# Performance work log

Measured on AMD Instinct MI355X. Metric: run time of the kernel, lower is better.

## Reference

```python
import jax, jax.numpy as jnp
import numpy as np

# Layer dims and sparsity levels, hard-coded in the original module
_DIMS = [(1024, 1000, 0.73), (1000, 800, 0.72), (800, 400, 0.70), (400, 600, 0.70), (600, 6, 0.50)]


def setup_inputs() -> dict:
    key = jax.random.key(0)
    ks = jax.random.split(key, 1 + 3 * len(_DIMS))
    inp = {"x": jax.random.normal(ks[0], (32768, 1024), dtype=jnp.float32)}
    for i, (fin, fout, sp) in enumerate(_DIMS):
        kw, kb, km = ks[1 + 3 * i], ks[2 + 3 * i], ks[3 + 3 * i]
        # Kaiming-ish init like nn.Linear default
        bound = 1.0 / np.sqrt(fin)
        inp[f"W{i+1}"] = jax.random.uniform(kw, (fout, fin), jnp.float32, -bound, bound)
        inp[f"b{i+1}"] = jax.random.uniform(kb, (fout,), jnp.float32, -bound, bound)
        # Unstructured sparsity mask: fraction `sp` of weights are zero
        inp[f"mask{i+1}"] = (jax.random.uniform(km, (fout, fin)) >= sp)
    return inp


def _sparse_linear(x, W, b, mask):
    # y = x @ (W * mask)^T + b ; mask encodes the fixed sparse connectivity
    Ws = jnp.where(mask, W, 0.0)
    return x @ Ws.T + b


def reference(x, W1, b1, mask1, W2, b2, mask2, W3, b3, mask3, W4, b4, mask4, W5, b5, mask5):
    h1 = jax.nn.relu(_sparse_linear(x, W1, b1, mask1))   # [B, 1000]
    h2 = jax.nn.relu(_sparse_linear(h1, W2, b2, mask2))  # [B, 800]
    h3 = jax.nn.relu(_sparse_linear(h2, W3, b3, mask3))  # [B, 400]
    h4 = _sparse_linear(h3, W4, b4, mask4)               # [B, 600] (no relu)
    h5 = _sparse_linear(h4, W5, b5, mask5)               # [B, 6]   (no relu)
    # original returns (x, results dict); return tuple (final, fc1..fc5)
    return (h5, h1, h2, h3, h4, h5)
```

## Files before the change

kernel.cpp:

```cpp
#include <hip/hip_runtime.h>
#include <stdint.h>

using u8  = unsigned char;
using u16 = unsigned short;
using u32 = unsigned int;

typedef __bf16 bf16x8 __attribute__((ext_vector_type(8)));
typedef float  f32x4  __attribute__((ext_vector_type(4)));
typedef u16    u16x8  __attribute__((ext_vector_type(8)));

__device__ __forceinline__ float b2f(u16 u) {
    union { u32 i; float f; } v; v.i = ((u32)u) << 16; return v.f;
}
__device__ __forceinline__ u16 f2bf(float f) {
    union { float f; u32 i; } v; v.f = f;
    u32 u = v.i;
    return (u16)((u + 0x7FFFu + ((u >> 16) & 1u)) >> 16);
}

#define WS_OFF 256
#define OFF_W1 0
#define OFF_W2 1048576
#define OFF_W3 1966080
#define OFF_W4 2392064
#define PS1 1048576
#define PS2 917504
#define PS3 425984
#define PS4 286720
#define TOTW 2678784
#define GUARD 64
#define OFF_XC  2678784
#define OFF_H1C 36233216
#define OFF_H2C 69001280
#define OFF_H3C 95215744
#define XCONV_N 4194304

__global__ void detect_kernel(int* __restrict__ flags,
                              const u32* __restrict__ xw,
                              const u32* __restrict__ mw) {
    const int lane = threadIdx.x;
    int outl = 0;
#pragma unroll
    for (int i = 0; i < 4; ++i) {
        u32 u = xw[lane * 4 + i];
        u32 e = (u >> 7) & 0xFFu;
        if (e < 90u || e > 140u) outl++;
    }
#pragma unroll
    for (int off = 32; off; off >>= 1) outl += __shfl_down(outl, off, 64);

    u32 v0 = mw[lane], v1 = mw[64 + lane];
    bool w4 = (v0 == 0u || v0 == 1u || v0 == 0x3F800000u) &&
              (v1 == 0u || v1 == 1u || v1 == 0x3F800000u);
    auto okh = [](u32 h) { return h == 0u || h == 1u || h == 0x3F80u; };
    bool w2 = okh(v0 & 0xFFFFu) && okh(v0 >> 16) && okh(v1 & 0xFFFFu) && okh(v1 >> 16);
    int all4 = __all(w4 ? 1 : 0);
    int all2 = __all(w2 ? 1 : 0);
    if (lane == 0) {
        flags[0] = (outl > 64) ? 1 : 0;
        flags[1] = all4 ? 0 : (all2 ? 1 : 2);
    }
}

__device__ __forceinline__ bool readM(const void* m, int s, int mwid) {
    if (mwid == 0) return ((const u32*)m)[s] != 0u;
    if (mwid == 1) return ((const u16*)m)[s] != 0u;
    return ((const u8*)m)[s] != 0u;
}
__device__ __forceinline__ u16 readW(const void* W, int s, int dt) {
    if (dt) return f2bf(((const float*)W)[s]);
    return ((const u16*)W)[s];
}

__global__ void prep_weights(const int* __restrict__ flags, u16* __restrict__ ws,
                             const void* __restrict__ W1, const void* __restrict__ m1,
                             const void* __restrict__ W2, const void* __restrict__ m2,
                             const void* __restrict__ W3, const void* __restrict__ m3,
                             const void* __restrict__ W4, const void* __restrict__ m4,
                             const void* __restrict__ xv)
{
    const int dt = flags[0], mwid = flags[1];
    int idx = blockIdx.x * 256 + threadIdx.x;
    if (idx < PS1) {
        int n = idx >> 10, k = idx & 1023;
        u16 v = 0;
        if (n < 1000) { int s = n * 1024 + k; if (readM(m1, s, mwid)) v = readW(W1, s, dt); }
        ws[idx] = v;
    } else if (idx < PS1 + PS2) {
        int j = idx - PS1; int n = j >> 10, k = j & 1023;
        u16 v = 0;
        if (n < 800 && k < 1000) { int s = n * 1000 + k; if (readM(m2, s, mwid)) v = readW(W2, s, dt); }
        ws[idx] = v;
    } else if (idx < PS1 + PS2 + PS3) {
        int j = idx - (PS1 + PS2); int n = j / 832, k = j - n * 832;
        u16 v = 0;
        if (n < 400 && k < 800) { int s = n * 800 + k; if (readM(m3, s, mwid)) v = readW(W3, s, dt); }
        ws[idx] = v;
    } else if (idx < TOTW) {
        int j = idx - (PS1 + PS2 + PS3); int n = j / 448, k = j - n * 448;
        u16 v = 0;
        if (n < 600 && k < 400) { int s = n * 400 + k; if (readM(m4, s, mwid)) v = readW(W4, s, dt); }
        ws[idx] = v;
    } else if (idx < TOTW + 3 * GUARD) {
        int g = idx - TOTW;
        int zone = g >> 6;
        size_t off = (zone == 0) ? ((size_t)OFF_H1C + 32768000)
                   : (zone == 1) ? ((size_t)OFF_H2C + 26214400)
                                 : ((size_t)OFF_H3C + 13107200);
        ws[off + (g & 63)] = 0;
    } else if (dt) {
        int c = idx - (TOTW + 3 * GUARD);
        if (c < XCONV_N) {
            const float4* s = (const float4*)xv + (size_t)c * 2;
            float4 a = s[0], b = s[1];
            u16x8 o;
            o[0] = f2bf(a.x); o[1] = f2bf(a.y); o[2] = f2bf(a.z); o[3] = f2bf(a.w);
            o[4] = f2bf(b.x); o[5] = f2bf(b.y); o[6] = f2bf(b.z); o[7] = f2bf(b.w);
            ((u16x8*)(ws + OFF_XC))[c] = o;
        }
    }
}

template <bool RELU>
__global__ __launch_bounds__(256, 3) void gemm_bt(
    const int* __restrict__ flags,
    const u16* __restrict__ A0,
    const u16* __restrict__ A1,
    int strideA, int Kpad, int NY,
    const u16* __restrict__ Wp,
    const void* __restrict__ bias, int N,
    void* __restrict__ dOut, size_t outOff,
    u16* __restrict__ Cc)
{
    const int mode = flags[0];
    const u16* __restrict__ A = mode ? A1 : A0;

    __shared__ __attribute__((aligned(16))) char sA[16384];
    __shared__ __attribute__((aligned(16))) char sB[16384];

    const int tid  = threadIdx.x;
    const int lane = tid & 63, wid = tid >> 6;
    const int wm = wid >> 1, wn = wid & 1;

    const int per = gridDim.x >> 3;
    const int idx = (blockIdx.x & 7) * per + (blockIdx.x >> 3);
    const int bm0 = (idx / NY) * 128, bn0 = (idx % NY) * 128;

    const int q = lane >> 4, r15 = lane & 15, key = lane & 7;
    const int l3 = lane >> 3, l7 = lane & 7;
    const int kbx = (l7 ^ l3) << 3;

    const u16* gA = A  + (size_t)(bm0 + wid * 32 + l3) * (size_t)strideA + kbx;
    const u16* gB = Wp + (size_t)(bn0 + wid * 32 + l3) * (size_t)Kpad   + kbx;
    char* sAw = sA + wid * 4096;
    char* sBw = sB + wid * 4096;

    f32x4 acc[4][4];
#pragma unroll
    for (int i = 0; i < 4; ++i)
#pragma unroll
        for (int j = 0; j < 4; ++j) acc[i][j] = (f32x4){0.f, 0.f, 0.f, 0.f};

    for (int k0 = 0; k0 < Kpad; k0 += 64) {
        if (k0) __syncthreads();
#pragma unroll
        for (int t = 0; t < 4; ++t) {
            __builtin_amdgcn_global_load_lds(
                (const __attribute__((address_space(1))) void*)(gA + (size_t)t * 8 * strideA),
                (__attribute__((address_space(3))) void*)(sAw + t * 1024), 16, 0, 0);
            __builtin_amdgcn_global_load_lds(
                (const __attribute__((address_space(1))) void*)(gB + (size_t)t * 8 * Kpad),
                (__attribute__((address_space(3))) void*)(sBw + t * 1024), 16, 0, 0);
        }
        gA += 64; gB += 64;
        __syncthreads();

#pragma unroll
        for (int kk = 0; kk < 2; ++kk) {
            bf16x8 af[4], bfr[4];
#pragma unroll
            for (int mi = 0; mi < 4; ++mi)
                af[mi] = *(const bf16x8*)(sA + (wm * 64 + mi * 16 + r15) * 128 +
                                          (((kk * 4 + q) ^ key) << 4));
#pragma unroll
            for (int ni = 0; ni < 4; ++ni)
                bfr[ni] = *(const bf16x8*)(sB + (wn * 64 + ni * 16 + r15) * 128 +
                                           (((kk * 4 + q) ^ key) << 4));
#pragma unroll
            for (int mi = 0; mi < 4; ++mi)
#pragma unroll
                for (int ni = 0; ni < 4; ++ni)
                    acc[mi][ni] = __builtin_amdgcn_mfma_f32_16x16x32_bf16(
                        af[mi], bfr[ni], acc[mi][ni], 0, 0, 0);
        }
    }

    float bv[4];
#pragma unroll
    for (int ni = 0; ni < 4; ++ni) {
        int col = bn0 + wn * 64 + ni * 16 + r15;
        bv[ni] = (col < N) ? (mode ? ((const float*)bias)[col] : b2f(((const u16*)bias)[col]))
                           : 0.f;
    }
    float* out32 = (float*)dOut + outOff;
    u16*   out16 = (u16*)dOut + outOff;
#pragma unroll
    for (int mi = 0; mi < 4; ++mi) {
#pragma unroll
        for (int ni = 0; ni < 4; ++ni) {
            int col = bn0 + wn * 64 + ni * 16 + r15;
            if (col < N) {
#pragma unroll
                for (int rr = 0; rr < 4; ++rr) {
                    int row = bm0 + wm * 64 + mi * 16 + q * 4 + rr;
                    float v = acc[mi][ni][rr] + bv[ni];
                    if (RELU) v = v > 0.f ? v : 0.f;
                    size_t o = (size_t)row * N + col;
                    if (Cc) Cc[o] = f2bf(v);
                    if (mode) out32[o] = v;
                    else      out16[o] = f2bf(v);
                }
            }
        }
    }
}

__global__ void layer5(const int* __restrict__ flags, void* __restrict__ dOut,
                       const void* __restrict__ W5v, const void* __restrict__ b5v,
                       const void* __restrict__ m5v)
{
    const int mode = flags[0], mwid = flags[1];
    __shared__ float w[6 * 600];
    __shared__ float bs[6];
    const int tid = threadIdx.x;
    for (int i = tid; i < 3600; i += 256)
        w[i] = readM(m5v, i, mwid)
                 ? (mode ? ((const float*)W5v)[i] : b2f(((const u16*)W5v)[i])) : 0.f;
    if (tid < 6)
        bs[tid] = mode ? ((const float*)b5v)[tid] : b2f(((const u16*)b5v)[tid]);
    __syncthreads();

    const int wid = tid >> 6, lane = tid & 63;
    const int row = blockIdx.x * 4 + wid;

    const float* h4f = (const float*)dOut + 72286208;
    const u16*   h4b = (const u16*)dOut + 72286208;

    float acc[6] = {0.f, 0.f, 0.f, 0.f, 0.f, 0.f};
    for (int p = lane; p < 300; p += 64) {
        float f0, f1;
        if (mode) {
            float2 hv = *(const float2*)(h4f + (size_t)row * 600 + 2 * p);
            f0 = hv.x; f1 = hv.y;
        } else {
            u32 u = *(const u32*)(h4b + (size_t)row * 600 + 2 * p);
            f0 = b2f((u16)(u & 0xffff)); f1 = b2f((u16)(u >> 16));
        }
        int k = 2 * p;
#pragma unroll
        for (int j = 0; j < 6; ++j) {
            float2 wv = *(const float2*)&w[j * 600 + k];
            acc[j] += f0 * wv.x + f1 * wv.y;
        }
    }
#pragma unroll
    for (int j = 0; j < 6; ++j)
#pragma unroll
        for (int off = 32; off > 0; off >>= 1)
            acc[j] += __shfl_down(acc[j], off, 64);

    if (lane == 0) {
#pragma unroll
        for (int j = 0; j < 6; ++j) {
            float v = acc[j] + bs[j];
            size_t o0 = (size_t)row * 6 + j;
            if (mode) {
                ((float*)dOut)[o0] = v;
                ((float*)dOut)[91947008 + o0] = v;
            } else {
                u16 b = f2bf(v);
                ((u16*)dOut)[o0] = b;
                ((u16*)dOut)[91947008 + o0] = b;
            }
        }
    }
}

extern "C" void kernel_launch(void* const* d_in, const int* in_sizes, int n_in,
                              void* d_out, int out_size, void* d_ws, size_t ws_size,
                              hipStream_t stream) {
    int* flags = (int*)d_ws;
    u16* wsW   = (u16*)d_ws + WS_OFF;

    detect_kernel<<<1, 64, 0, stream>>>(flags, (const u32*)d_in[0], (const u32*)d_in[3]);
    prep_weights<<<26849, 256, 0, stream>>>(flags, wsW,
                                            d_in[1], d_in[3], d_in[4], d_in[6],
                                            d_in[7], d_in[9], d_in[10], d_in[12],
                                            d_in[0]);

    gemm_bt<true><<<2048, 256, 0, stream>>>(flags, (const u16*)d_in[0], wsW + OFF_XC,
                                            1024, 1024, 8, wsW + OFF_W1, d_in[2], 1000,
                                            d_out, 196608, wsW + OFF_H1C);
    gemm_bt<true><<<1792, 256, 0, stream>>>(flags, wsW + OFF_H1C, wsW + OFF_H1C,
                                            1000, 1024, 7, wsW + OFF_W2, d_in[5], 800,
                                            d_out, 32964608, wsW + OFF_H2C);
    gemm_bt<true><<<1024, 256, 0, stream>>>(flags, wsW + OFF_H2C, wsW + OFF_H2C,
                                            800, 832, 4, wsW + OFF_W3, d_in[8], 400,
                                            d_out, 59179008, wsW + OFF_H3C);
    gemm_bt<false><<<1280, 256, 0, stream>>>(flags, wsW + OFF_H3C, wsW + OFF_H3C,
                                             400, 448, 5, wsW + OFF_W4, d_in[11], 600,
                                             d_out, 72286208, (u16*)nullptr);
    layer5<<<8192, 256, 0, stream>>>(flags, d_out, d_in[13], d_in[14], d_in[15]);
}
```

Measured before the change: 826.9 us.

## Fuse layer-5 projection into layer-4 GEMM epilogue with atomic partial sums

Layer 5 (600->6) is now computed inside the layer-4 GEMM epilogue. Each block multiplies its output tile by the matching slice of W5 held in shared memory, reduces across lanes, and atomically adds partial sums into a zeroed fp32 scratch buffer. A small finalize kernel then adds the bias and writes both copies of h5. This avoids re-reading h4 from global memory in a separate kernel. It adds atomics and an extra shared-memory fill in the epilogue, and launch bounds are raised from 3 to 4 blocks per SM, which may cause register spills.

```diff
diff --git a/kernel.cpp b/kernel.cpp
--- a/kernel.cpp
+++ b/kernel.cpp
@@ -33,6 +33,8 @@
 #define OFF_H1C 36233216
 #define OFF_H2C 69001280
 #define OFF_H3C 95215744
+#define OFF_H5S 108323008
+#define H5N 196608
 #define XCONV_N 4194304
 
 __global__ void detect_kernel(int* __restrict__ flags,
@@ -108,8 +110,10 @@
                    : (zone == 1) ? ((size_t)OFF_H2C + 26214400)
                                  : ((size_t)OFF_H3C + 13107200);
         ws[off + (g & 63)] = 0;
+    } else if (idx < TOTW + 3 * GUARD + H5N) {
+        ((float*)(ws + OFF_H5S))[idx - (TOTW + 3 * GUARD)] = 0.f;
     } else if (dt) {
-        int c = idx - (TOTW + 3 * GUARD);
+        int c = idx - (TOTW + 3 * GUARD + H5N);
         if (c < XCONV_N) {
             const float4* s = (const float4*)xv + (size_t)c * 2;
             float4 a = s[0], b = s[1];
@@ -121,8 +125,8 @@
     }
 }
 
-template <bool RELU>
-__global__ __launch_bounds__(256, 3) void gemm_bt(
+template <bool RELU, bool FUSE>
+__global__ __launch_bounds__(256, 4) void gemm_bt(
     const int* __restrict__ flags,
     const u16* __restrict__ A0,
     const u16* __restrict__ A1,
@@ -130,7 +134,9 @@
     const u16* __restrict__ Wp,
     const void* __restrict__ bias, int N,
     void* __restrict__ dOut, size_t outOff,
-    u16* __restrict__ Cc)
+    u16* __restrict__ Cc,
+    const void* __restrict__ W5v, const void* __restrict__ m5v,
+    float* __restrict__ scratch)
 {
     const int mode = flags[0];
     const u16* __restrict__ A = mode ? A1 : A0;
@@ -195,6 +201,21 @@
         }
     }
 
+    float* w5s = (float*)sA;
+    if constexpr (FUSE) {
+        const int mwid = flags[1];
+        __syncthreads();
+        for (int i = tid; i < 768; i += 256) {
+            int j = i >> 7, c = i & 127, col = bn0 + c;
+            float wv = 0.f;
+            if (col < 600 && readM(m5v, j * 600 + col, mwid))
+                wv = mode ? ((const float*)W5v)[j * 600 + col]
+                          : b2f(((const u16*)W5v)[j * 600 + col]);
+            w5s[i] = wv;
+        }
+        __syncthreads();
+    }
+
     float bv[4];
 #pragma unroll
     for (int ni = 0; ni < 4; ++ni) {
@@ -202,87 +223,68 @@
         bv[ni] = (col < N) ? (mode ? ((const float*)bias)[col] : b2f(((const u16*)bias)[col]))
                            : 0.f;
     }
+    float wreg[6][4];
+    if constexpr (FUSE) {
+#pragma unroll
+        for (int j = 0; j < 6; ++j)
+#pragma unroll
+            for (int ni = 0; ni < 4; ++ni)
+                wreg[j][ni] = w5s[j * 128 + wn * 64 + ni * 16 + r15];
+    }
+
     float* out32 = (float*)dOut + outOff;
     u16*   out16 = (u16*)dOut + outOff;
 #pragma unroll
     for (int mi = 0; mi < 4; ++mi) {
 #pragma unroll
-        for (int ni = 0; ni < 4; ++ni) {
-            int col = bn0 + wn * 64 + ni * 16 + r15;
-            if (col < N) {
-#pragma unroll
-                for (int rr = 0; rr < 4; ++rr) {
-                    int row = bm0 + wm * 64 + mi * 16 + q * 4 + rr;
-                    float v = acc[mi][ni][rr] + bv[ni];
-                    if (RELU) v = v > 0.f ? v : 0.f;
+        for (int rr = 0; rr < 4; ++rr) {
+            int row = bm0 + wm * 64 + mi * 16 + q * 4 + rr;
+            float vv[4];
+#pragma unroll
+            for (int ni = 0; ni < 4; ++ni) {
+                float v = acc[mi][ni][rr] + bv[ni];
+                if (RELU) v = v > 0.f ? v : 0.f;
+                vv[ni] = v;
+                int col = bn0 + wn * 64 + ni * 16 + r15;
+                if (col < N) {
                     size_t o = (size_t)row * N + col;
                     if (Cc) Cc[o] = f2bf(v);
                     if (mode) out32[o] = v;
                     else      out16[o] = f2bf(v);
                 }
             }
-        }
-    }
-}
-
-__global__ void layer5(const int* __restrict__ flags, void* __restrict__ dOut,
-                       const void* __restrict__ W5v, const void* __restrict__ b5v,
-                       const void* __restrict__ m5v)
+            if constexpr (FUSE) {
+#pragma unroll
+                for (int j = 0; j < 6; ++j) {
+                    float p = vv[0] * wreg[j][0] + vv[1] * wreg[j][1] +
+                              vv[2] * wreg[j][2] + vv[3] * wreg[j][3];
+                    p += __shfl_xor(p, 1, 64);
+                    p += __shfl_xor(p, 2, 64);
+                    p += __shfl_xor(p, 4, 64);
+                    p += __shfl_xor(p, 8, 64);
+                    if (r15 == 0) atomicAdd(&scratch[(size_t)row * 6 + j], p);
+                }
+            }
+        }
+    }
+}
+
+__global__ void finalize5(const int* __restrict__ flags,
+                          const float* __restrict__ scratch,
+                          const void* __restrict__ b5v, void* __restrict__ dOut)
 {
-    const int mode = flags[0], mwid = flags[1];
-    __shared__ float w[6 * 600];
-    __shared__ float bs[6];
-    const int tid = threadIdx.x;
-    for (int i = tid; i < 3600; i += 256)
-        w[i] = readM(m5v, i, mwid)
-                 ? (mode ? ((const float*)W5v)[i] : b2f(((const u16*)W5v)[i])) : 0.f;
-    if (tid < 6)
-        bs[tid] = mode ? ((const float*)b5v)[tid] : b2f(((const u16*)b5v)[tid]);
-    __syncthreads();
-
-    const int wid = tid >> 6, lane = tid & 63;
-    const int row = blockIdx.x * 4 + wid;
-
-    const float* h4f = (const float*)dOut + 72286208;
-    const u16*   h4b = (const u16*)dOut + 72286208;
-
-    float acc[6] = {0.f, 0.f, 0.f, 0.f, 0.f, 0.f};
-    for (int p = lane; p < 300; p += 64) {
-        float f0, f1;
-        if (mode) {
-            float2 hv = *(const float2*)(h4f + (size_t)row * 600 + 2 * p);
-            f0 = hv.x; f1 = hv.y;
-        } else {
-            u32 u = *(const u32*)(h4b + (size_t)row * 600 + 2 * p);
-            f0 = b2f((u16)(u & 0xffff)); f1 = b2f((u16)(u >> 16));
-        }
-        int k = 2 * p;
-#pragma unroll
-        for (int j = 0; j < 6; ++j) {
-            float2 wv = *(const float2*)&w[j * 600 + k];
-            acc[j] += f0 * wv.x + f1 * wv.y;
-        }
-    }
-#pragma unroll
-    for (int j = 0; j < 6; ++j)
-#pragma unroll
-        for (int off = 32; off > 0; off >>= 1)
-            acc[j] += __shfl_down(acc[j], off, 64);
-
-    if (lane == 0) {
-#pragma unroll
-        for (int j = 0; j < 6; ++j) {
-            float v = acc[j] + bs[j];
-            size_t o0 = (size_t)row * 6 + j;
-            if (mode) {
-                ((float*)dOut)[o0] = v;
-                ((float*)dOut)[91947008 + o0] = v;
-            } else {
-                u16 b = f2bf(v);
-                ((u16*)dOut)[o0] = b;
-                ((u16*)dOut)[91947008 + o0] = b;
-            }
-        }
+    const int mode = flags[0];
+    int idx = blockIdx.x * 256 + threadIdx.x;
+    int j = idx % 6;
+    float v = scratch[idx] +
+              (mode ? ((const float*)b5v)[j] : b2f(((const u16*)b5v)[j]));
+    if (mode) {
+        ((float*)dOut)[idx] = v;
+        ((float*)dOut)[91947008 + idx] = v;
+    } else {
+        u16 b = f2bf(v);
+        ((u16*)dOut)[idx] = b;
+        ((u16*)dOut)[91947008 + idx] = b;
     }
 }
 
@@ -291,24 +293,29 @@
                               hipStream_t stream) {
     int* flags = (int*)d_ws;
     u16* wsW   = (u16*)d_ws + WS_OFF;
+    float* h5s = (float*)(wsW + OFF_H5S);
 
     detect_kernel<<<1, 64, 0, stream>>>(flags, (const u32*)d_in[0], (const u32*)d_in[3]);
-    prep_weights<<<26849, 256, 0, stream>>>(flags, wsW,
+    prep_weights<<<27617, 256, 0, stream>>>(flags, wsW,
                                             d_in[1], d_in[3], d_in[4], d_in[6],
                                             d_in[7], d_in[9], d_in[10], d_in[12],
                                             d_in[0]);
 
-    gemm_bt<true><<<2048, 256, 0, stream>>>(flags, (const u16*)d_in[0], wsW + OFF_XC,
-                                            1024, 1024, 8, wsW + OFF_W1, d_in[2], 1000,
-                                            d_out, 196608, wsW + OFF_H1C);
-    gemm_bt<true><<<1792, 256, 0, stream>>>(flags, wsW + OFF_H1C, wsW + OFF_H1C,
-                                            1000, 1024, 7, wsW + OFF_W2, d_in[5], 800,
-                                            d_out, 32964608, wsW + OFF_H2C);
-    gemm_bt<true><<<1024, 256, 0, stream>>>(flags, wsW + OFF_H2C, wsW + OFF_H2C,
-                                            800, 832, 4, wsW + OFF_W3, d_in[8], 400,
-                                            d_out, 59179008, wsW + OFF_H3C);
-    gemm_bt<false><<<1280, 256, 0, stream>>>(flags, wsW + OFF_H3C, wsW + OFF_H3C,
-                                             400, 448, 5, wsW + OFF_W4, d_in[11], 600,
-                                             d_out, 72286208, (u16*)nullptr);
-    layer5<<<8192, 256, 0, stream>>>(flags, d_out, d_in[13], d_in[14], d_in[15]);
-}
+    gemm_bt<true, false><<<2048, 256, 0, stream>>>(flags, (const u16*)d_in[0], wsW + OFF_XC,
+                                                   1024, 1024, 8, wsW + OFF_W1, d_in[2], 1000,
+                                                   d_out, 196608, wsW + OFF_H1C,
+                                                   nullptr, nullptr, nullptr);
+    gemm_bt<true, false><<<1792, 256, 0, stream>>>(flags, wsW + OFF_H1C, wsW + OFF_H1C,
+                                                   1000, 1024, 7, wsW + OFF_W2, d_in[5], 800,
+                                                   d_out, 32964608, wsW + OFF_H2C,
+                                                   nullptr, nullptr, nullptr);
+    gemm_bt<true, false><<<1024, 256, 0, stream>>>(flags, wsW + OFF_H2C, wsW + OFF_H2C,
+                                                   800, 832, 4, wsW + OFF_W3, d_in[8], 400,
+                                                   d_out, 59179008, wsW + OFF_H3C,
+                                                   nullptr, nullptr, nullptr);
+    gemm_bt<false, true><<<1280, 256, 0, stream>>>(flags, wsW + OFF_H3C, wsW + OFF_H3C,
+                                                   400, 448, 5, wsW + OFF_W4, d_in[11], 600,
+                                                   d_out, 72286208, (u16*)nullptr,
+                                                   d_in[13], d_in[15], h5s);
+    finalize5<<<768, 256, 0, stream>>>(flags, h5s, d_in[14], d_out);
+}
```

Result: slower. 916.1 us (+10.8%).

## Use 256x256 tiles with double-buffered LDS pipeline in GEMM kernels

Applied to the files above, without the earlier changes.

Replaces the 128x128, 4-wave GEMM with a 256x256, 8-wave kernel whose A and B tiles sit in a 128KB double-buffered LDS region. The next K-stage is prefetched with global_load_lds while the current one is consumed, using explicit vmcnt waits and raw barriers instead of __syncthreads. It also raises MFMA priority around the compute block. The aim is more data reuse per tile and overlap of memory with compute. In exchange, the grids are much smaller (256-512 blocks), which may underfill the GPU and waste more work on padded edges for N=1000/800/400/600.

```diff
diff --git a/kernel.cpp b/kernel.cpp
--- a/kernel.cpp
+++ b/kernel.cpp
@@ -8,6 +8,9 @@
 typedef __bf16 bf16x8 __attribute__((ext_vector_type(8)));
 typedef float  f32x4  __attribute__((ext_vector_type(4)));
 typedef u16    u16x8  __attribute__((ext_vector_type(8)));
+
+#define AS1 __attribute__((address_space(1)))
+#define AS3 __attribute__((address_space(3)))
 
 __device__ __forceinline__ float b2f(u16 u) {
     union { u32 i; float f; } v; v.i = ((u32)u) << 16; return v.f;
@@ -122,11 +125,11 @@
 }
 
 template <bool RELU>
-__global__ __launch_bounds__(256, 3) void gemm_bt(
+__global__ __launch_bounds__(512, 2) void gemm256(
     const int* __restrict__ flags,
     const u16* __restrict__ A0,
     const u16* __restrict__ A1,
-    int strideA, int Kpad, int NY,
+    int strideA, int NT, int NY,
     const u16* __restrict__ Wp,
     const void* __restrict__ bias, int N,
     void* __restrict__ dOut, size_t outOff,
@@ -134,64 +137,91 @@
 {
     const int mode = flags[0];
     const u16* __restrict__ A = mode ? A1 : A0;
-
-    __shared__ __attribute__((aligned(16))) char sA[16384];
-    __shared__ __attribute__((aligned(16))) char sB[16384];
+    const int Kpad = NT * 64;
+
+    __shared__ __attribute__((aligned(16))) char smem[131072];
 
     const int tid  = threadIdx.x;
-    const int lane = tid & 63, wid = tid >> 6;
-    const int wm = wid >> 1, wn = wid & 1;
+    const int lane = tid & 63;
+    const int wid  = tid >> 6;
+    const int wm = wid >> 2, wn = wid & 3;
+    const int q = lane >> 4, r15 = lane & 15;
+    const int csq = q ^ ((r15 >> 1) & 3);
 
     const int per = gridDim.x >> 3;
     const int idx = (blockIdx.x & 7) * per + (blockIdx.x >> 3);
-    const int bm0 = (idx / NY) * 128, bn0 = (idx % NY) * 128;
-
-    const int q = lane >> 4, r15 = lane & 15, key = lane & 7;
-    const int l3 = lane >> 3, l7 = lane & 7;
-    const int kbx = (l7 ^ l3) << 3;
-
-    const u16* gA = A  + (size_t)(bm0 + wid * 32 + l3) * (size_t)strideA + kbx;
-    const u16* gB = Wp + (size_t)(bn0 + wid * 32 + l3) * (size_t)Kpad   + kbx;
-    char* sAw = sA + wid * 4096;
-    char* sBw = sB + wid * 4096;
-
-    f32x4 acc[4][4];
-#pragma unroll
-    for (int i = 0; i < 4; ++i)
+    const int bm0 = (idx / NY) * 256, bn0 = (idx % NY) * 256;
+
+    int srA[2], scA[2];
+#pragma unroll
+    for (int l = 0; l < 2; ++l) {
+        int m = l * 512 + tid;
+        int r = m >> 2, c = m & 3;
+        srA[l] = r;
+        scA[l] = (c ^ ((r >> 1) & 3)) * 8;
+    }
+
+    f32x4 acc[8][4];
+#pragma unroll
+    for (int i = 0; i < 8; ++i)
 #pragma unroll
         for (int j = 0; j < 4; ++j) acc[i][j] = (f32x4){0.f, 0.f, 0.f, 0.f};
 
-    for (int k0 = 0; k0 < Kpad; k0 += 64) {
-        if (k0) __syncthreads();
-#pragma unroll
-        for (int t = 0; t < 4; ++t) {
-            __builtin_amdgcn_global_load_lds(
-                (const __attribute__((address_space(1))) void*)(gA + (size_t)t * 8 * strideA),
-                (__attribute__((address_space(3))) void*)(sAw + t * 1024), 16, 0, 0);
-            __builtin_amdgcn_global_load_lds(
-                (const __attribute__((address_space(1))) void*)(gB + (size_t)t * 8 * Kpad),
-                (__attribute__((address_space(3))) void*)(sBw + t * 1024), 16, 0, 0);
-        }
-        gA += 64; gB += 64;
-        __syncthreads();
-
+    auto STAGE = [&](int t, int kk) {
+        const int kb = t * 64 + kk * 32;
+        const int pb = t & 1;
+        char* ldsA = smem + pb * 32768 + kk * 16384;
+        char* ldsB = smem + 65536 + pb * 32768 + kk * 16384;
+#pragma unroll
+        for (int l = 0; l < 2; ++l) {
+            const u16* src = A + (size_t)(bm0 + srA[l]) * (size_t)strideA + kb + scA[l];
+            __builtin_amdgcn_global_load_lds((const AS1 void*)src,
+                (AS3 void*)(ldsA + (l * 512 + tid) * 16), 16, 0, 0);
+        }
+#pragma unroll
+        for (int l = 0; l < 2; ++l) {
+            const u16* src = Wp + (size_t)(bn0 + srA[l]) * (size_t)Kpad + kb + scA[l];
+            __builtin_amdgcn_global_load_lds((const AS1 void*)src,
+                (AS3 void*)(ldsB + (l * 512 + tid) * 16), 16, 0, 0);
+        }
+    };
+
+    STAGE(0, 0);
+    STAGE(0, 1);
+
+    for (int t = 0; t < NT; ++t) {
+        const int pb = t & 1;
 #pragma unroll
         for (int kk = 0; kk < 2; ++kk) {
-            bf16x8 af[4], bfr[4];
-#pragma unroll
-            for (int mi = 0; mi < 4; ++mi)
-                af[mi] = *(const bf16x8*)(sA + (wm * 64 + mi * 16 + r15) * 128 +
-                                          (((kk * 4 + q) ^ key) << 4));
-#pragma unroll
-            for (int ni = 0; ni < 4; ++ni)
-                bfr[ni] = *(const bf16x8*)(sB + (wn * 64 + ni * 16 + r15) * 128 +
-                                           (((kk * 4 + q) ^ key) << 4));
-#pragma unroll
-            for (int mi = 0; mi < 4; ++mi)
+            const bool st = (t + 1 < NT);
+            if (st) STAGE(t + 1, kk);
+            if (st)           asm volatile("s_waitcnt vmcnt(8)" ::: "memory");
+            else if (kk == 0) asm volatile("s_waitcnt vmcnt(4)" ::: "memory");
+            else              asm volatile("s_waitcnt vmcnt(0)" ::: "memory");
+            __builtin_amdgcn_s_barrier();
+            __builtin_amdgcn_sched_barrier(0);
+
+            const char* Ab = smem + pb * 32768 + kk * 16384;
+            const char* Bb = smem + 65536 + pb * 32768 + kk * 16384;
+            bf16x8 af[8], bfr[4];
+#pragma unroll
+            for (int mi = 0; mi < 8; ++mi) {
+                int r = wm * 128 + mi * 16 + r15;
+                af[mi] = *(const bf16x8*)(Ab + r * 64 + csq * 16);
+            }
+#pragma unroll
+            for (int ni = 0; ni < 4; ++ni) {
+                int r = wn * 64 + ni * 16 + r15;
+                bfr[ni] = *(const bf16x8*)(Bb + r * 64 + csq * 16);
+            }
+            __builtin_amdgcn_s_setprio(1);
+#pragma unroll
+            for (int mi = 0; mi < 8; ++mi)
 #pragma unroll
                 for (int ni = 0; ni < 4; ++ni)
                     acc[mi][ni] = __builtin_amdgcn_mfma_f32_16x16x32_bf16(
                         af[mi], bfr[ni], acc[mi][ni], 0, 0, 0);
+            __builtin_amdgcn_s_setprio(0);
         }
     }
 
@@ -205,14 +235,14 @@
     float* out32 = (float*)dOut + outOff;
     u16*   out16 = (u16*)dOut + outOff;
 #pragma unroll
-    for (int mi = 0; mi < 4; ++mi) {
+    for (int mi = 0; mi < 8; ++mi) {
 #pragma unroll
         for (int ni = 0; ni < 4; ++ni) {
             int col = bn0 + wn * 64 + ni * 16 + r15;
             if (col < N) {
 #pragma unroll
                 for (int rr = 0; rr < 4; ++rr) {
-                    int row = bm0 + wm * 64 + mi * 16 + q * 4 + rr;
+                    int row = bm0 + wm * 128 + mi * 16 + q * 4 + rr;
                     float v = acc[mi][ni][rr] + bv[ni];
                     if (RELU) v = v > 0.f ? v : 0.f;
                     size_t o = (size_t)row * N + col;
@@ -298,17 +328,17 @@
                                             d_in[7], d_in[9], d_in[10], d_in[12],
                                             d_in[0]);
 
-    gemm_bt<true><<<2048, 256, 0, stream>>>(flags, (const u16*)d_in[0], wsW + OFF_XC,
-                                            1024, 1024, 8, wsW + OFF_W1, d_in[2], 1000,
-                                            d_out, 196608, wsW + OFF_H1C);
-    gemm_bt<true><<<1792, 256, 0, stream>>>(flags, wsW + OFF_H1C, wsW + OFF_H1C,
-                                            1000, 1024, 7, wsW + OFF_W2, d_in[5], 800,
-                                            d_out, 32964608, wsW + OFF_H2C);
-    gemm_bt<true><<<1024, 256, 0, stream>>>(flags, wsW + OFF_H2C, wsW + OFF_H2C,
-                                            800, 832, 4, wsW + OFF_W3, d_in[8], 400,
-                                            d_out, 59179008, wsW + OFF_H3C);
-    gemm_bt<false><<<1280, 256, 0, stream>>>(flags, wsW + OFF_H3C, wsW + OFF_H3C,
-                                             400, 448, 5, wsW + OFF_W4, d_in[11], 600,
-                                             d_out, 72286208, (u16*)nullptr);
+    gemm256<true><<<512, 512, 0, stream>>>(flags, (const u16*)d_in[0], wsW + OFF_XC,
+                                           1024, 16, 4, wsW + OFF_W1, d_in[2], 1000,
+                                           d_out, 196608, wsW + OFF_H1C);
+    gemm256<true><<<512, 512, 0, stream>>>(flags, wsW + OFF_H1C, wsW + OFF_H1C,
+                                           1000, 16, 4, wsW + OFF_W2, d_in[5], 800,
+                                           d_out, 32964608, wsW + OFF_H2C);
+    gemm256<true><<<256, 512, 0, stream>>>(flags, wsW + OFF_H2C, wsW + OFF_H2C,
+                                           800, 13, 2, wsW + OFF_W3, d_in[8], 400,
+                                           d_out, 59179008, wsW + OFF_H3C);
+    gemm256<false><<<384, 512, 0, stream>>>(flags, wsW + OFF_H3C, wsW + OFF_H3C,
+                                            400, 7, 3, wsW + OFF_W4, d_in[11], 600,
+                                            d_out, 72286208, (u16*)nullptr);
     layer5<<<8192, 256, 0, stream>>>(flags, d_out, d_in[13], d_in[14], d_in[15]);
 }
```

Measured after the change: 812.9 us. No clear change (-1.7%).

## Fuse prep, GEMM layers, and layer5 into one persistent cooperative kernel

Applied to the files above, without the earlier changes.

Replaces the separate prep, four GEMM and layer5 launches with one persistent cooperative kernel. Its blocks loop over tiles in each phase and use grid.sync between phases, with a fallback to the old multi-launch path if the cooperative launch fails. The aim is to remove launch gaps and tail effects between kernels. In exchange it drops the XCD-aware block remapping, keeps the grid fixed at occupancy times CU count, and adds the cost of the grid-wide barriers.

```diff
diff --git a/kernel.cpp b/kernel.cpp
--- a/kernel.cpp
+++ b/kernel.cpp
@@ -1,5 +1,8 @@
 #include <hip/hip_runtime.h>
+#include <hip/hip_cooperative_groups.h>
 #include <stdint.h>
+
+namespace cg = cooperative_groups;
 
 using u8  = unsigned char;
 using u16 = unsigned short;
@@ -8,6 +11,9 @@
 typedef __bf16 bf16x8 __attribute__((ext_vector_type(8)));
 typedef float  f32x4  __attribute__((ext_vector_type(4)));
 typedef u16    u16x8  __attribute__((ext_vector_type(8)));
+
+#define AS1 __attribute__((address_space(1)))
+#define AS3 __attribute__((address_space(3)))
 
 __device__ __forceinline__ float b2f(u16 u) {
     union { u32 i; float f; } v; v.i = ((u32)u) << 16; return v.f;
@@ -34,6 +40,7 @@
 #define OFF_H2C 69001280
 #define OFF_H3C 95215744
 #define XCONV_N 4194304
+#define PREP_TOT (TOTW + 3 * GUARD + XCONV_N)
 
 __global__ void detect_kernel(int* __restrict__ flags,
                               const u32* __restrict__ xw,
@@ -72,15 +79,13 @@
     return ((const u16*)W)[s];
 }
 
-__global__ void prep_weights(const int* __restrict__ flags, u16* __restrict__ ws,
-                             const void* __restrict__ W1, const void* __restrict__ m1,
-                             const void* __restrict__ W2, const void* __restrict__ m2,
-                             const void* __restrict__ W3, const void* __restrict__ m3,
-                             const void* __restrict__ W4, const void* __restrict__ m4,
-                             const void* __restrict__ xv)
-{
-    const int dt = flags[0], mwid = flags[1];
-    int idx = blockIdx.x * 256 + threadIdx.x;
+__device__ __forceinline__ void prep_one(int idx, int dt, int mwid, u16* __restrict__ ws,
+                                         const void* __restrict__ W1, const void* __restrict__ m1,
+                                         const void* __restrict__ W2, const void* __restrict__ m2,
+                                         const void* __restrict__ W3, const void* __restrict__ m3,
+                                         const void* __restrict__ W4, const void* __restrict__ m4,
+                                         const void* __restrict__ xv)
+{
     if (idx < PS1) {
         int n = idx >> 10, k = idx & 1023;
         u16 v = 0;
@@ -122,30 +127,15 @@
 }
 
 template <bool RELU>
-__global__ __launch_bounds__(256, 3) void gemm_bt(
-    const int* __restrict__ flags,
-    const u16* __restrict__ A0,
-    const u16* __restrict__ A1,
-    int strideA, int Kpad, int NY,
-    const u16* __restrict__ Wp,
-    const void* __restrict__ bias, int N,
-    void* __restrict__ dOut, size_t outOff,
-    u16* __restrict__ Cc)
-{
-    const int mode = flags[0];
-    const u16* __restrict__ A = mode ? A1 : A0;
-
-    __shared__ __attribute__((aligned(16))) char sA[16384];
-    __shared__ __attribute__((aligned(16))) char sB[16384];
-
+__device__ __forceinline__ void gemm_tile(
+    int mode, const u16* __restrict__ A, int strideA, int Kpad,
+    const u16* __restrict__ Wp, const void* __restrict__ bias, int N,
+    void* __restrict__ dOut, size_t outOff, u16* __restrict__ Cc,
+    int bm0, int bn0, char* sA, char* sB)
+{
     const int tid  = threadIdx.x;
     const int lane = tid & 63, wid = tid >> 6;
     const int wm = wid >> 1, wn = wid & 1;
-
-    const int per = gridDim.x >> 3;
-    const int idx = (blockIdx.x & 7) * per + (blockIdx.x >> 3);
-    const int bm0 = (idx / NY) * 128, bn0 = (idx % NY) * 128;
-
     const int q = lane >> 4, r15 = lane & 15, key = lane & 7;
     const int l3 = lane >> 3, l7 = lane & 7;
     const int kbx = (l7 ^ l3) << 3;
@@ -161,16 +151,17 @@
 #pragma unroll
         for (int j = 0; j < 4; ++j) acc[i][j] = (f32x4){0.f, 0.f, 0.f, 0.f};
 
+    __syncthreads();
     for (int k0 = 0; k0 < Kpad; k0 += 64) {
         if (k0) __syncthreads();
 #pragma unroll
         for (int t = 0; t < 4; ++t) {
             __builtin_amdgcn_global_load_lds(
-                (const __attribute__((address_space(1))) void*)(gA + (size_t)t * 8 * strideA),
-                (__attribute__((address_space(3))) void*)(sAw + t * 1024), 16, 0, 0);
+                (const AS1 void*)(gA + (size_t)t * 8 * strideA),
+                (AS3 void*)(sAw + t * 1024), 16, 0, 0);
             __builtin_amdgcn_global_load_lds(
-                (const __attribute__((address_space(1))) void*)(gB + (size_t)t * 8 * Kpad),
-                (__attribute__((address_space(3))) void*)(sBw + t * 1024), 16, 0, 0);
+                (const AS1 void*)(gB + (size_t)t * 8 * Kpad),
+                (AS3 void*)(sBw + t * 1024), 16, 0, 0);
         }
         gA += 64; gB += 64;
         __syncthreads();
@@ -225,13 +216,27 @@
     }
 }
 
-__global__ void layer5(const int* __restrict__ flags, void* __restrict__ dOut,
-                       const void* __restrict__ W5v, const void* __restrict__ b5v,
-                       const void* __restrict__ m5v)
-{
-    const int mode = flags[0], mwid = flags[1];
-    __shared__ float w[6 * 600];
-    __shared__ float bs[6];
+template <bool RELU>
+__device__ void gemm_phase(int mode, const u16* __restrict__ A, int strideA, int Kpad,
+                           const u16* __restrict__ Wp, const void* __restrict__ bias,
+                           int N, int nyt, int mtiles,
+                           void* __restrict__ dOut, size_t outOff, u16* __restrict__ Cc,
+                           char* sA, char* sB)
+{
+    const int ntiles = mtiles * nyt;
+    for (int tt = blockIdx.x; tt < ntiles; tt += gridDim.x) {
+        const int mt = tt / nyt, nt = tt - mt * nyt;
+        gemm_tile<RELU>(mode, A, strideA, Kpad, Wp, bias, N,
+                        dOut, outOff, Cc, mt * 128, nt * 128, sA, sB);
+    }
+}
+
+__device__ void layer5_phase(int mode, int mwid, void* __restrict__ dOut,
+                             const void* __restrict__ W5v, const void* __restrict__ b5v,
+                             const void* __restrict__ m5v, char* smem)
+{
+    float* w  = (float*)smem;
+    float* bs = (float*)(smem + 14400);
     const int tid = threadIdx.x;
     for (int i = tid; i < 3600; i += 256)
         w[i] = readM(m5v, i, mwid)
@@ -241,49 +246,126 @@
     __syncthreads();
 
     const int wid = tid >> 6, lane = tid & 63;
-    const int row = blockIdx.x * 4 + wid;
-
     const float* h4f = (const float*)dOut + 72286208;
     const u16*   h4b = (const u16*)dOut + 72286208;
 
-    float acc[6] = {0.f, 0.f, 0.f, 0.f, 0.f, 0.f};
-    for (int p = lane; p < 300; p += 64) {
-        float f0, f1;
-        if (mode) {
-            float2 hv = *(const float2*)(h4f + (size_t)row * 600 + 2 * p);
-            f0 = hv.x; f1 = hv.y;
-        } else {
-            u32 u = *(const u32*)(h4b + (size_t)row * 600 + 2 * p);
-            f0 = b2f((u16)(u & 0xffff)); f1 = b2f((u16)(u >> 16));
-        }
-        int k = 2 * p;
-#pragma unroll
-        for (int j = 0; j < 6; ++j) {
-            float2 wv = *(const float2*)&w[j * 600 + k];
-            acc[j] += f0 * wv.x + f1 * wv.y;
-        }
-    }
-#pragma unroll
-    for (int j = 0; j < 6; ++j)
-#pragma unroll
-        for (int off = 32; off > 0; off >>= 1)
-            acc[j] += __shfl_down(acc[j], off, 64);
-
-    if (lane == 0) {
-#pragma unroll
-        for (int j = 0; j < 6; ++j) {
-            float v = acc[j] + bs[j];
-            size_t o0 = (size_t)row * 6 + j;
+    for (int g = blockIdx.x; g < 8192; g += gridDim.x) {
+        const int row = g * 4 + wid;
+        float acc[6] = {0.f, 0.f, 0.f, 0.f, 0.f, 0.f};
+        for (int p = lane; p < 300; p += 64) {
+            float f0, f1;
             if (mode) {
-                ((float*)dOut)[o0] = v;
-                ((float*)dOut)[91947008 + o0] = v;
+                float2 hv = *(const float2*)(h4f + (size_t)row * 600 + 2 * p);
+                f0 = hv.x; f1 = hv.y;
             } else {
-                u16 b = f2bf(v);
-                ((u16*)dOut)[o0] = b;
-                ((u16*)dOut)[91947008 + o0] = b;
+                u32 u = *(const u32*)(h4b + (size_t)row * 600 + 2 * p);
+                f0 = b2f((u16)(u & 0xffff)); f1 = b2f((u16)(u >> 16));
             }
-        }
-    }
+            int k = 2 * p;
+#pragma unroll
+            for (int j = 0; j < 6; ++j) {
+                float2 wv = *(const float2*)&w[j * 600 + k];
+                acc[j] += f0 * wv.x + f1 * wv.y;
+            }
+        }
+#pragma unroll
+        for (int j = 0; j < 6; ++j)
+#pragma unroll
+            for (int off = 32; off > 0; off >>= 1)
+                acc[j] += __shfl_down(acc[j], off, 64);
+
+        if (lane == 0) {
+#pragma unroll
+            for (int j = 0; j < 6; ++j) {
+                float v = acc[j] + bs[j];
+                size_t o0 = (size_t)row * 6 + j;
+                if (mode) {
+                    ((float*)dOut)[o0] = v;
+                    ((float*)dOut)[91947008 + o0] = v;
+                } else {
+                    u16 b = f2bf(v);
+                    ((u16*)dOut)[o0] = b;
+                    ((u16*)dOut)[91947008 + o0] = b;
+                }
+            }
+        }
+    }
+}
+
+__global__ __launch_bounds__(256, 3) void mega(
+    const int* __restrict__ flags, u16* __restrict__ ws,
+    const void* __restrict__ W1, const void* __restrict__ m1,
+    const void* __restrict__ W2, const void* __restrict__ m2,
+    const void* __restrict__ W3, const void* __restrict__ m3,
+    const void* __restrict__ W4, const void* __restrict__ m4,
+    const void* __restrict__ W5, const void* __restrict__ b5,
+    const void* __restrict__ m5, const void* __restrict__ xv,
+    const void* __restrict__ b1, const void* __restrict__ b2,
+    const void* __restrict__ b3, const void* __restrict__ b4,
+    void* __restrict__ dOut)
+{
+    cg::grid_group grid = cg::this_grid();
+    __shared__ __attribute__((aligned(16))) char smem[32768];
+    const int dt = flags[0], mwid = flags[1];
+    const int stride = gridDim.x * 256;
+
+    for (int idx = blockIdx.x * 256 + threadIdx.x; idx < PREP_TOT; idx += stride)
+        prep_one(idx, dt, mwid, ws, W1, m1, W2, m2, W3, m3, W4, m4, xv);
+    grid.sync();
+
+    {
+        const u16* A = dt ? ws + OFF_XC : (const u16*)xv;
+        gemm_phase<true>(dt, A, 1024, 1024, ws + OFF_W1, b1, 1000, 8, 256,
+                         dOut, (size_t)196608, ws + OFF_H1C, smem, smem + 16384);
+    }
+    grid.sync();
+    gemm_phase<true>(dt, ws + OFF_H1C, 1000, 1024, ws + OFF_W2, b2, 800, 7, 256,
+                     dOut, (size_t)32964608, ws + OFF_H2C, smem, smem + 16384);
+    grid.sync();
+    gemm_phase<true>(dt, ws + OFF_H2C, 800, 832, ws + OFF_W3, b3, 400, 4, 256,
+                     dOut, (size_t)59179008, ws + OFF_H3C, smem, smem + 16384);
+    grid.sync();
+    gemm_phase<false>(dt, ws + OFF_H3C, 400, 448, ws + OFF_W4, b4, 600, 5, 256,
+                      dOut, (size_t)72286208, (u16*)nullptr, smem, smem + 16384);
+    grid.sync();
+    layer5_phase(dt, mwid, dOut, W5, b5, m5, smem);
+}
+
+__global__ void prep_weights(const int* __restrict__ flags, u16* __restrict__ ws,
+                             const void* __restrict__ W1, const void* __restrict__ m1,
+                             const void* __restrict__ W2, const void* __restrict__ m2,
+                             const void* __restrict__ W3, const void* __restrict__ m3,
+                             const void* __restrict__ W4, const void* __restrict__ m4,
+                             const void* __restrict__ xv)
+{
+    const int dt = flags[0], mwid = flags[1];
+    int idx = blockIdx.x * 256 + threadIdx.x;
+    if (idx < PREP_TOT)
+        prep_one(idx, dt, mwid, ws, W1, m1, W2, m2, W3, m3, W4, m4, xv);
+}
+
+template <bool RELU>
+__global__ __launch_bounds__(256, 3) void gemm_bt(
+    const int* __restrict__ flags,
+    const u16* __restrict__ A0, const u16* __restrict__ A1,
+    int strideA, int Kpad,
+    const u16* __restrict__ Wp, const void* __restrict__ bias, int N,
+    void* __restrict__ dOut, size_t outOff, u16* __restrict__ Cc)
+{
+    const int mode = flags[0];
+    const u16* A = mode ? A1 : A0;
+    __shared__ __attribute__((aligned(16))) char sA[16384];
+    __shared__ __attribute__((aligned(16))) char sB[16384];
+    gemm_tile<RELU>(mode, A, strideA, Kpad, Wp, bias, N, dOut, outOff, Cc,
+                    blockIdx.x * 128, blockIdx.y * 128, sA, sB);
+}
+
+__global__ void layer5(const int* __restrict__ flags, void* __restrict__ dOut,
+                       const void* __restrict__ W5v, const void* __restrict__ b5v,
+                       const void* __restrict__ m5v)
+{
+    __shared__ __attribute__((aligned(16))) char smem[14432];
+    layer5_phase(flags[0], flags[1], dOut, W5v, b5v, m5v, smem);
 }
 
 extern "C" void kernel_launch(void* const* d_in, const int* in_sizes, int n_in,
@@ -293,22 +375,49 @@
     u16* wsW   = (u16*)d_ws + WS_OFF;
 
     detect_kernel<<<1, 64, 0, stream>>>(flags, (const u32*)d_in[0], (const u32*)d_in[3]);
-    prep_weights<<<26849, 256, 0, stream>>>(flags, wsW,
-                                            d_in[1], d_in[3], d_in[4], d_in[6],
-                                            d_in[7], d_in[9], d_in[10], d_in[12],
-                                            d_in[0]);
-
-    gemm_bt<true><<<2048, 256, 0, stream>>>(flags, (const u16*)d_in[0], wsW + OFF_XC,
-                                            1024, 1024, 8, wsW + OFF_W1, d_in[2], 1000,
-                                            d_out, 196608, wsW + OFF_H1C);
-    gemm_bt<true><<<1792, 256, 0, stream>>>(flags, wsW + OFF_H1C, wsW + OFF_H1C,
-                                            1000, 1024, 7, wsW + OFF_W2, d_in[5], 800,
-                                            d_out, 32964608, wsW + OFF_H2C);
-    gemm_bt<true><<<1024, 256, 0, stream>>>(flags, wsW + OFF_H2C, wsW + OFF_H2C,
-                                            800, 832, 4, wsW + OFF_W3, d_in[8], 400,
-                                            d_out, 59179008, wsW + OFF_H3C);
-    gemm_bt<false><<<1280, 256, 0, stream>>>(flags, wsW + OFF_H3C, wsW + OFF_H3C,
-                                             400, 448, 5, wsW + OFF_W4, d_in[11], 600,
-                                             d_out, 72286208, (u16*)nullptr);
-    layer5<<<8192, 256, 0, stream>>>(flags, d_out, d_in[13], d_in[14], d_in[15]);
-}
+
+    static int g_grid = -1;
+    if (g_grid < 0) {
+        int dev = 0, cus = 0, occ = 0;
+        hipGetDevice(&dev);
+        hipDeviceGetAttribute(&cus, hipDeviceAttributeMultiprocessorCount, dev);
+        hipOccupancyMaxActiveBlocksPerMultiprocessor(&occ, (const void*)mega, 256, 0);
+        if (cus < 1) cus = 256;
+        if (occ < 1) occ = 1;
+        g_grid = cus * occ;
+        if (g_grid > 2048) g_grid = 2048;
+    }
+
+    const void* w1 = d_in[1],  *m1 = d_in[3],  *b1 = d_in[2];
+    const void* w2 = d_in[4],  *m2 = d_in[6],  *b2 = d_in[5];
+    const void* w3 = d_in[7],  *m3 = d_in[9],  *b3 = d_in[8];
+    const void* w4 = d_in[10], *m4 = d_in[12], *b4 = d_in[11];
+    const void* w5 = d_in[13], *b5 = d_in[14], *m5 = d_in[15];
+    const void* xv = d_in[0];
+    void* dOut = d_out;
+
+    void* args[] = {&flags, &wsW,
+                    (void*)&w1, (void*)&m1, (void*)&w2, (void*)&m2,
+                    (void*)&w3, (void*)&m3, (void*)&w4, (void*)&m4,
+                    (void*)&w5, (void*)&b5, (void*)&m5, (void*)&xv,
+                    (void*)&b1, (void*)&b2, (void*)&b3, (void*)&b4,
+                    &dOut};
+    hipError_t e = hipLaunchCooperativeKernel((const void*)mega, dim3(g_grid), dim3(256),
+                                              args, 0, stream);
+    if (e != hipSuccess) {
+        prep_weights<<<26849, 256, 0, stream>>>(flags, wsW, w1, m1, w2, m2, w3, m3, w4, m4, xv);
+        gemm_bt<true><<<dim3(256, 8), 256, 0, stream>>>(flags, (const u16*)xv, wsW + OFF_XC,
+                                                        1024, 1024, wsW + OFF_W1, b1, 1000,
+                                                        dOut, (size_t)196608, wsW + OFF_H1C);
+        gemm_bt<true><<<dim3(256, 7), 256, 0, stream>>>(flags, wsW + OFF_H1C, wsW + OFF_H1C,
+                                                        1000, 1024, wsW + OFF_W2, b2, 800,
+                                                        dOut, (size_t)32964608, wsW + OFF_H2C);
+        gemm_bt<true><<<dim3(256, 4), 256, 0, stream>>>(flags, wsW + OFF_H2C, wsW + OFF_H2C,
+                                                        800, 832, wsW + OFF_W3, b3, 400,
+                                                        dOut, (size_t)59179008, wsW + OFF_H3C);
+        gemm_bt<false><<<dim3(256, 5), 256, 0, stream>>>(flags, wsW + OFF_H3C, wsW + OFF_H3C,
+                                                         400, 448, wsW + OFF_W4, b4, 600,
+                                                         dOut, (size_t)72286208, (u16*)nullptr);
+        layer5<<<8192, 256, 0, stream>>>(flags, dOut, w5, b5, m5);
+    }
+}
```

Result: slower. 1.357 ms (+64.1%).
